# Performance work log

Hardware: AMD Instinct MI355X
Metric: run time of the kernel (lower is better)

## Reference

```python
import jax, jax.numpy as jnp
import numpy as np

C_IN = 512      # backbone feature dim (din)
CORR = 256      # cfg.SIAMESE.NUM_CHANNELS_FOR_CORRELATION
EXPAND = 64     # expand_factor
N_ANCH = 9      # 3 scales x 3 ratios
KH = 7          # template spatial size
H = W = 32      # target feature map size
N_T = 2         # number of templates
BN_EPS = 1e-5


def _conv(x, w, b=None, pad=0, groups=1):
    out = jax.lax.conv_general_dilated(
        x, w, window_strides=(1, 1), padding=[(pad, pad), (pad, pad)],
        dimension_numbers=('NCHW', 'OIHW', 'NCHW'), feature_group_count=groups)
    if b is not None:
        out = out + b[None, :, None, None]
    return out


def setup_inputs() -> dict:
    key = jax.random.key(0)
    ks = jax.random.split(key, 10)
    return {
        'target_feat': jax.random.normal(ks[0], (1, C_IN, H, W), jnp.float32),
        'template_feat': jax.random.normal(ks[1], (N_T, C_IN, KH, KH), jnp.float32),
        'w_target': jax.random.normal(ks[2], (CORR, C_IN, 3, 3), jnp.float32) * 0.01,
        'b_target': jnp.zeros((CORR,), jnp.float32),
        'bn_gamma': jnp.ones((CORR,), jnp.float32),
        'bn_beta': jnp.zeros((CORR,), jnp.float32),
        'bn_mean': jax.random.normal(ks[3], (CORR,), jnp.float32) * 0.1,
        'bn_var': jax.random.uniform(ks[4], (CORR,), jnp.float32, 0.5, 1.5),
        'w_template': jax.random.normal(ks[5], (CORR * EXPAND, C_IN, 3, 3), jnp.float32) * 0.01,
        'b_template': jnp.zeros((CORR * EXPAND,), jnp.float32),
        'w_merge_cls': jax.random.normal(ks[6], (CORR,), jnp.float32) * 0.01,
        'corr_bias': jnp.zeros((EXPAND, 1, 1), jnp.float32),
        'w_cls': jax.random.normal(ks[7], (2 * N_ANCH, EXPAND, 1, 1), jnp.float32) * 0.01,
        'b_cls': jnp.zeros((2 * N_ANCH,), jnp.float32),
        'w_box': jax.random.normal(ks[8], (4 * N_ANCH, EXPAND, 1, 1), jnp.float32) * 0.001,
        'b_box': jnp.zeros((4 * N_ANCH,), jnp.float32),
    }


def reference(target_feat, template_feat, w_target, b_target, bn_gamma, bn_beta,
              bn_mean, bn_var, w_template, b_template, w_merge_cls, corr_bias,
              w_cls, b_cls, w_box, b_box):
    N = template_feat.shape[0]
    Hh, Ww = target_feat.shape[2], target_feat.shape[3]
    # RPN_Conv_target (3x3, pad 1) + BatchNorm (eval mode, running stats)
    t = _conv(target_feat, w_target, b_target, pad=1)               # (1, CORR, H, W)
    scale = (bn_gamma / jnp.sqrt(bn_var + BN_EPS))[None, :, None, None]
    t = (t - bn_mean[None, :, None, None]) * scale + bn_beta[None, :, None, None]
    # RPN_Conv_template (3x3, pad 1) on template features
    z = _conv(template_feat, w_template, b_template, pad=1)          # (N, CORR*EXPAND, kh, kw)
    kh, kw = z.shape[2], z.shape[3]
    # depth-wise cross correlation: kernel (N*EXPAND*CORR, 1, kh, kw), groups=CORR
    kern = z.reshape(N * EXPAND * CORR, 1, kh, kw)
    out = 0.1 * _conv(t, kern, pad=(kh - 1) // 2, groups=CORR)       # (1, N*EXPAND*CORR, H, W)
    out = out.reshape(N * EXPAND, CORR, Hh, Ww)
    # conv_merge_1x1_cls: 1x1 conv CORR -> 1, no bias
    out = jnp.einsum('nchw,c->nhw', out, w_merge_cls)                # (N*EXPAND, H, W)
    rpn_feat = out.reshape(N, EXPAND, Hh, Ww) + corr_bias[None]      # (N, 64, H, W)
    # cls / bbox heads (1x1 convs)
    cls = _conv(rpn_feat, w_cls, b_cls)                              # (N, 18, H, W)
    box = _conv(rpn_feat, w_box, b_box)                              # (N, 36, H, W)
    nc = cls.shape[1]
    # reshape to (N, 2, A*H, W), softmax over dim 1, reshape back
    prob = jax.nn.softmax(cls.reshape(N, 2, (nc // 2) * Hh, Ww), axis=1)
    prob = prob.reshape(N, nc, Hh, Ww)
    return prob, box
```

## Files before the change

### kernel.cpp

```cpp
#include <hip/hip_runtime.h>
#include <math.h>


#define WS_TFP 0
#define WS_TP  591872
#define WS_BF  980992
#define WS_WFP 981120
#define WS_Z2P 2160768
#define WS_MRG 2562176
#define WS_CVP 2693248
#define WFP_HALF 589824

typedef float f4u __attribute__((ext_vector_type(4), aligned(4)));
typedef float f4a __attribute__((ext_vector_type(4)));

#define FMA4(ww, vv) \
  acc.x = fmaf(ww, (vv).x, acc.x); acc.y = fmaf(ww, (vv).y, acc.y); \
  acc.z = fmaf(ww, (vv).z, acc.z); acc.w = fmaf(ww, (vv).w, acc.w)

__global__ __launch_bounds__(256) void k0_prep(
    const float* __restrict__ tfeat,
    const float* __restrict__ wm,
    const float* __restrict__ btpl,
    float* ws)
{
  const int N0 = 591872, N2 = 389120;
  const int total = N0 + N2;
  for (int idx = blockIdx.x * 256 + threadIdx.x; idx < total + 128; idx += gridDim.x * 256) {
    if (idx < N0) {
      int ci = idx / 1156, r = idx % 1156;
      int yy = r / 34, xx = r % 34;
      float v = 0.f;
      if (yy >= 1 && yy <= 32 && xx >= 1 && xx <= 32)
        v = tfeat[ci * 1024 + (yy - 1) * 32 + (xx - 1)];
      ws[WS_TFP + idx] = v;
    } else if (idx < total) {
      ws[WS_TP + (idx - N0)] = 0.f;
    } else {
      const int eh = idx - total;
      const int e = eh >> 1, h = eh & 1;
      const float* wmp = wm + h * 128;
      const float* bp = btpl + e * 256 + h * 128;
      float s = 0.f;
      for (int cl = 0; cl < 128; cl++) s = fmaf(wmp[cl], bp[cl], s);
      ws[WS_BF + eh] = s;
    }
  }
}

__global__ __launch_bounds__(256, 8) void K1_fold_conv(
    const float* __restrict__ wtpl,
    const float* __restrict__ wm,
    const float* __restrict__ wtgt,
    float* ws)
{
  const int bid0 = blockIdx.x;
  const int tid = threadIdx.x;
  const int q = bid0 / 17, r17 = bid0 % 17;
  if (r17 < 9) {
    const int fi = q * 9 + r17;
    const int g = fi / 18, rest = fi % 18;
    const int chunk = rest >> 1, half = rest & 1;
    const int colv = tid & 127, rowg = tid >> 7;
    const int c0 = chunk * 512 + colv * 4;
    const int row0 = g * 128 + half * 64 + rowg * 32;
    const float* base = wtpl + (size_t)row0 * 4608 + c0;
    const float* wmb = wm + (g & 1) * 128 + half * 64 + rowg * 32;
    f4a acc = {0.f, 0.f, 0.f, 0.f};
    for (int rr = 0; rr < 32; rr += 8) {
      const float* b = base + (size_t)rr * 4608;
      const f4a v0 = *(const f4a*)(b);
      const f4a v1 = *(const f4a*)(b + 1 * 4608);
      const f4a v2 = *(const f4a*)(b + 2 * 4608);
      const f4a v3 = *(const f4a*)(b + 3 * 4608);
      const f4a v4 = *(const f4a*)(b + 4 * 4608);
      const f4a v5 = *(const f4a*)(b + 5 * 4608);
      const f4a v6 = *(const f4a*)(b + 6 * 4608);
      const f4a v7 = *(const f4a*)(b + 7 * 4608);
      const float w0 = wmb[rr + 0], w1 = wmb[rr + 1];
      const float w2 = wmb[rr + 2], w3 = wmb[rr + 3];
      const float w4 = wmb[rr + 4], w5 = wmb[rr + 5];
      const float w6 = wmb[rr + 6], w7 = wmb[rr + 7];
      FMA4(w0, v0); FMA4(w1, v1); FMA4(w2, v2); FMA4(w3, v3);
      FMA4(w4, v4); FMA4(w5, v5); FMA4(w6, v6); FMA4(w7, v7);
    }
    __shared__ f4a red[128];
    if (rowg) red[colv] = acc;
    __syncthreads();
    if (!rowg) {
      const f4a o = red[colv];
      acc.x += o.x; acc.y += o.y; acc.z += o.z; acc.w += o.w;
      float* wp = ws + WS_WFP + (size_t)half * WFP_HALF + (size_t)g * 4608;
      *(f4a*)(wp + c0) = acc;
    }
  } else {
    const int bid = q * 8 + (r17 - 9);
    const int coblk = bid >> 7, pxblk = (bid >> 3) & 15, ks = bid & 7;
    const int ksub = tid >> 7, sub = tid & 127;
    const int cog = sub >> 5, pxg = sub & 31;
    const int row = pxg >> 4, x0 = (pxg & 15) * 2;
    const int y = pxblk * 2 + row;
    const int co0 = coblk * 16 + cog * 4;
    const int ci0 = ks * 64 + ksub * 32;
    const float* tfp = ws + WS_TFP;

    float acc[4][2] = {{0.f, 0.f}, {0.f, 0.f}, {0.f, 0.f}, {0.f, 0.f}};
    for (int i = 0; i < 32; i++) {
      const int ci = ci0 + i;
      const float* tin = tfp + (size_t)ci * 1156 + y * 34 + x0;
      const f4u p0 = *(const f4u*)(tin);
      const f4u p1 = *(const f4u*)(tin + 34);
      const f4u p2 = *(const f4u*)(tin + 68);
      #pragma unroll
      for (int c = 0; c < 4; c++) {
        const float* wr = wtgt + (size_t)(co0 + c) * 4608 + ci * 9;
        const f4u wa = *(const f4u*)(wr);
        const f4u wb = *(const f4u*)(wr + 4);
        const float w8 = wr[8];
        acc[c][0] += wa.x * p0.x + wa.y * p0.y + wa.z * p0.z
                   + wa.w * p1.x + wb.x * p1.y + wb.y * p1.z
                   + wb.z * p2.x + wb.w * p2.y + w8 * p2.z;
        acc[c][1] += wa.x * p0.y + wa.y * p0.z + wa.z * p0.w
                   + wa.w * p1.y + wb.x * p1.z + wb.y * p1.w
                   + wb.z * p2.y + wb.w * p2.z + w8 * p2.w;
      }
    }
    float* cvp = ws + WS_CVP + (size_t)(ks * 2 + ksub) * 262144;
    #pragma unroll
    for (int c = 0; c < 4; c++) {
      cvp[(co0 + c) * 1024 + y * 32 + x0 + 0] = acc[c][0];
      cvp[(co0 + c) * 1024 + y * 32 + x0 + 1] = acc[c][1];
    }
  }
}

__global__ __launch_bounds__(256) void K2_cred_z2(
    const float* __restrict__ btgt,
    const float* __restrict__ gamma, const float* __restrict__ beta,
    const float* __restrict__ mean, const float* __restrict__ var,
    const float* __restrict__ zfeat,
    float* ws)
{
  __shared__ float Tl[50][144];
  const int tid = threadIdx.x;
  if (blockIdx.x < 256) {
    const int co = blockIdx.x;
    const float sc = gamma[co] * rsqrtf(var[co] + 1e-5f);
    const float off = btgt[co] - mean[co];
    const float bt = beta[co];
    const float* cvp = ws + WS_CVP + (size_t)co * 1024;
    float* tP = ws + WS_TP;
    #pragma unroll
    for (int k = 0; k < 4; k++) {
      const int j = k * 256 + tid;
      float s = 0.f;
      #pragma unroll
      for (int sl = 0; sl < 16; sl++) s += cvp[(size_t)sl * 262144 + j];
      const float t = ((s + off) * sc + bt) * 0.1f;
      const int yy = j >> 5, xx = j & 31;
      tP[co * 1520 + (yy + 3) * 40 + (xx + 3)] = t;
    }
  } else {
    const int b2 = blockIdx.x - 256;
    const int n = b2 >> 5, kc = b2 & 31;
    const int ci0 = kc * 16;
    for (int idx = tid; idx < 7200; idx += 256) {
      const int uv = idx / 144, kk = idx % 144;
      float v = 0.f;
      if (uv < 49) {
        const int u = uv / 7, vv = uv % 7;
        const int ci = ci0 + kk / 9, pq = kk % 9;
        const int p = pq / 3, q2 = pq % 3;
        const int yy = u + p - 1, xx = vv + q2 - 1;
        if (yy >= 0 && yy < 7 && xx >= 0 && xx < 7)
          v = zfeat[n * 25088 + ci * 49 + yy * 7 + xx];
      }
      Tl[uv][kk] = v;
    }
    __syncthreads();
    const int ehq = tid & 31, uvg = tid >> 5;
    const int eh0 = ehq * 4;
    const int uv0 = (uvg == 0) ? 0 : uvg * 6 + 1;
    const float* wfp = ws + WS_WFP;
    float4 acc[7];
    #pragma unroll
    for (int i = 0; i < 7; i++) acc[i] = make_float4(0.f, 0.f, 0.f, 0.f);
    for (int g = 0; g < 36; g++) {
      const int koff = ci0 * 9 + g * 4;
      f4a wvE[4];
      #pragma unroll
      for (int e = 0; e < 4; e++) {
        const float* pe = wfp + (size_t)(eh0 + e) * 4608 + koff;
        f4a a = *(const f4a*)(pe);
        a += *(const f4a*)(pe + WFP_HALF);
        wvE[e] = a;
      }
      #pragma unroll
      for (int uu = 0; uu < 7; uu++) {
        const float4 t4 = *(const float4*)(&Tl[uv0 + uu][g * 4]);
        acc[uu].x = fmaf(t4.x, wvE[0].x, fmaf(t4.y, wvE[0].y, fmaf(t4.z, wvE[0].z, fmaf(t4.w, wvE[0].w, acc[uu].x))));
        acc[uu].y = fmaf(t4.x, wvE[1].x, fmaf(t4.y, wvE[1].y, fmaf(t4.z, wvE[1].z, fmaf(t4.w, wvE[1].w, acc[uu].y))));
        acc[uu].z = fmaf(t4.x, wvE[2].x, fmaf(t4.y, wvE[2].y, fmaf(t4.z, wvE[2].z, fmaf(t4.w, wvE[2].w, acc[uu].z))));
        acc[uu].w = fmaf(t4.x, wvE[3].x, fmaf(t4.y, wvE[3].y, fmaf(t4.z, wvE[3].z, fmaf(t4.w, wvE[3].w, acc[uu].w))));
      }
    }
    float* z2p = ws + WS_Z2P;
    #pragma unroll
    for (int uu = 0; uu < 7; uu++) {
      const int uv = uv0 + uu;
      if (uv <= 48)
        *(float4*)(z2p + ((size_t)((n * 32 + kc) * 49 + uv)) * 128 + eh0) = acc[uu];
    }
  }
}

__global__ __launch_bounds__(128) void k3_merged(float* ws)
{
  __shared__ float Z2s[16][7][8];
  const int tid = threadIdx.x;
  const int bid = blockIdx.x;
  const int n = bid >> 7, rest = bid & 127;
  const int ec = rest >> 4, hq = rest & 15;
  const int c0 = ec * 16, h0 = hq * 2;
  const float* z2p = ws + WS_Z2P;
  const float* bf = ws + WS_BF;
  for (int idx = tid; idx < 784; idx += 128) {
    const int cl = idx & 15, uv = idx >> 4;
    float s = bf[c0 + cl];
    const float* p = z2p + (size_t)(n * 1568 + uv) * 128 + (c0 + cl);
    #pragma unroll 8
    for (int kc = 0; kc < 32; kc++) s += p[(size_t)kc * 6272];
    Z2s[cl][uv / 7][uv % 7] = s;
  }
  for (int idx = tid; idx < 112; idx += 128)
    Z2s[idx / 7][idx % 7][7] = 0.f;
  __syncthreads();

  const int e = tid >> 4, row = (tid >> 3) & 1, wq = tid & 7;
  const int w0 = wq * 4;
  const float* tP = ws + WS_TP;
  float acc[4] = {0.f, 0.f, 0.f, 0.f};
  #pragma unroll
  for (int h128 = 0; h128 < 2; h128++) {
    const int cl = 2 * e + h128;
    const float* tc = tP + (size_t)(128 * n + c0 + cl) * 1520;
    #pragma unroll
    for (int u = 0; u < 7; u++) {
      const float* trow = tc + (h0 + row + u) * 40 + w0;
      float tw[12];
      *(float4*)&tw[0] = *(const float4*)(trow);
      *(float4*)&tw[4] = *(const float4*)(trow + 4);
      *(float4*)&tw[8] = *(const float4*)(trow + 8);
      float z[8];
      *(float4*)&z[0] = *(const float4*)&Z2s[cl][u][0];
      *(float4*)&z[4] = *(const float4*)&Z2s[cl][u][4];
      #pragma unroll
      for (int px = 0; px < 4; px++)
        #pragma unroll
        for (int v = 0; v < 8; v++)
          acc[px] = fmaf(z[v], tw[px + v], acc[px]);
    }
  }
  float* mrg = ws + WS_MRG;
  *(float4*)(mrg + (size_t)(((n * 64 + ec * 8 + e) * 32) + h0 + row) * 32 + w0) =
      make_float4(acc[0], acc[1], acc[2], acc[3]);
}

__global__ __launch_bounds__(256) void k4_heads(
    const float* __restrict__ cb,
    const float* __restrict__ wcls, const float* __restrict__ bcls,
    const float* __restrict__ wbox, const float* __restrict__ bbox,
    float* ws, float* __restrict__ out)
{
  __shared__ float mrg_l[32][66];
  __shared__ float wcb_l[54][64];
  __shared__ float bias_l[54];
  __shared__ float logits[18][32];
  const int tid = threadIdx.x;
  const int n = blockIdx.x >> 5, h = blockIdx.x & 31;
  const float* mrg = ws + WS_MRG;
  for (int idx = tid; idx < 2048; idx += 256) {
    const int e = idx >> 5, w = idx & 31;
    mrg_l[w][e] = mrg[(size_t)(((n * 64 + e) * 32) + h) * 32 + w] + cb[e];
  }
  for (int idx = tid; idx < 3456; idx += 256) {
    const int ch = idx >> 6, e = idx & 63;
    wcb_l[ch][e] = (ch < 18) ? wcls[ch * 64 + e] : wbox[(ch - 18) * 64 + e];
  }
  if (tid < 54) bias_l[tid] = (tid < 18) ? bcls[tid] : bbox[tid - 18];
  __syncthreads();

  const int w = tid & 31, chg = tid >> 5;
  const int cnt = (chg < 6) ? 7 : 6;
  float acc[7] = {0.f, 0.f, 0.f, 0.f, 0.f, 0.f, 0.f};
  for (int e2 = 0; e2 < 32; e2++) {
    const float2 m2 = *(const float2*)&mrg_l[w][e2 * 2];
    #pragma unroll
    for (int i = 0; i < 7; i++) {
      if (i < cnt) {
        const int ch = chg + 8 * i;
        const float2 wv = *(const float2*)&wcb_l[ch][e2 * 2];
        acc[i] = fmaf(m2.x, wv.x, acc[i]);
        acc[i] = fmaf(m2.y, wv.y, acc[i]);
      }
    }
  }
  #pragma unroll
  for (int i = 0; i < 7; i++) {
    if (i < cnt) {
      const int ch = chg + 8 * i;
      const float v = acc[i] + bias_l[ch];
      if (ch < 18) logits[ch][w] = v;
      else out[36864 + n * 36864 + (ch - 18) * 1024 + h * 32 + w] = v;
    }
  }
  __syncthreads();
  for (int idx = tid; idx < 576; idx += 256) {
    const int ch = idx >> 5, w2 = idx & 31;
    const float a = logits[ch][w2];
    const float b = logits[(ch + 9) % 18][w2];
    const float m = fmaxf(a, b);
    const float ea = expf(a - m), eb = expf(b - m);
    out[n * 18432 + ch * 1024 + h * 32 + w2] = ea / (ea + eb);
  }
}

extern "C" void kernel_launch(void* const* d_in, const int* in_sizes, int n_in,
                              void* d_out, int out_size, void* d_ws, size_t ws_size,
                              hipStream_t stream) {
  (void)in_sizes; (void)n_in; (void)out_size; (void)ws_size;
  const float* target_feat   = (const float*)d_in[0];
  const float* template_feat = (const float*)d_in[1];
  const float* w_target      = (const float*)d_in[2];
  const float* b_target      = (const float*)d_in[3];
  const float* bn_gamma      = (const float*)d_in[4];
  const float* bn_beta       = (const float*)d_in[5];
  const float* bn_mean       = (const float*)d_in[6];
  const float* bn_var        = (const float*)d_in[7];
  const float* w_template    = (const float*)d_in[8];
  const float* b_template    = (const float*)d_in[9];
  const float* w_merge       = (const float*)d_in[10];
  const float* corr_bias     = (const float*)d_in[11];
  const float* w_cls         = (const float*)d_in[12];
  const float* b_cls         = (const float*)d_in[13];
  const float* w_box         = (const float*)d_in[14];
  const float* b_box         = (const float*)d_in[15];
  float* ws = (float*)d_ws;
  float* out = (float*)d_out;

  hipLaunchKernelGGL(k0_prep, dim3(2048), dim3(256), 0, stream,
                     target_feat, w_merge, b_template, ws);
  hipLaunchKernelGGL(K1_fold_conv, dim3(4352), dim3(256), 0, stream,
                     w_template, w_merge, w_target, ws);
  hipLaunchKernelGGL(K2_cred_z2, dim3(320), dim3(256), 0, stream,
                     b_target, bn_gamma, bn_beta, bn_mean, bn_var,
                     template_feat, ws);
  hipLaunchKernelGGL(k3_merged, dim3(256), dim3(128), 0, stream, ws);
  hipLaunchKernelGGL(k4_heads, dim3(64), dim3(256), 0, stream,
                     corr_bias, w_cls, b_cls, w_box, b_box, ws, out);
}
```

Baseline: 240.2 us.

## Split fold into standalone wide kernel with 8 partial slabs and nontemporal loads

The template-weight fold that merges w_merge into w_template moves out of the combined fold/conv kernel into its own kernel. That kernel launches 9216 blocks, each reducing 16 rows and writing one of 8 partial slabs, where before fewer blocks each looped over 64 rows. The big weight stream now uses nontemporal loads, and the conv part becomes its own kernel. The goal is more memory-level parallelism on the large w_template read. In exchange, K2 must sum 8 slabs instead of 2 on every weight load, the workspace grows, and there is one more kernel launch.

```diff
diff --git a/kernel.cpp b/kernel.cpp
--- a/kernel.cpp
+++ b/kernel.cpp
@@ -6,10 +6,10 @@
 #define WS_TP  591872
 #define WS_BF  980992
 #define WS_WFP 981120
-#define WS_Z2P 2160768
-#define WS_MRG 2562176
-#define WS_CVP 2693248
-#define WFP_HALF 589824
+#define WS_Z2P 5699712
+#define WS_MRG 6101120
+#define WS_CVP 6232192
+#define WFP_SLAB 589824
 
 typedef float f4u __attribute__((ext_vector_type(4), aligned(4)));
 typedef float f4a __attribute__((ext_vector_type(4)));
@@ -17,6 +17,46 @@
 #define FMA4(ww, vv) \
   acc.x = fmaf(ww, (vv).x, acc.x); acc.y = fmaf(ww, (vv).y, acc.y); \
   acc.z = fmaf(ww, (vv).z, acc.z); acc.w = fmaf(ww, (vv).w, acc.w)
+
+#define NTL(p) __builtin_nontemporal_load((const f4a*)(p))
+
+__global__ __launch_bounds__(256) void k_fold(
+    const float* __restrict__ wtpl,
+    const float* __restrict__ wm,
+    float* ws)
+{
+  const int b = blockIdx.x;
+  const int g = b / 72, rest = b % 72;
+  const int chunk = rest / 8, rsub = rest % 8;
+  const int tid = threadIdx.x;
+  const int colv = tid & 127, rowg = tid >> 7;
+  const int c0 = chunk * 512 + colv * 4;
+  const int row0 = g * 128 + rsub * 16 + rowg * 8;
+  const float* base = wtpl + (size_t)row0 * 4608 + c0;
+  const float* wmb = wm + (g & 1) * 128 + rsub * 16 + rowg * 8;
+  f4a acc = {0.f, 0.f, 0.f, 0.f};
+  const f4a v0 = NTL(base);
+  const f4a v1 = NTL(base + 1 * 4608);
+  const f4a v2 = NTL(base + 2 * 4608);
+  const f4a v3 = NTL(base + 3 * 4608);
+  const f4a v4 = NTL(base + 4 * 4608);
+  const f4a v5 = NTL(base + 5 * 4608);
+  const f4a v6 = NTL(base + 6 * 4608);
+  const f4a v7 = NTL(base + 7 * 4608);
+  const float w0 = wmb[0], w1 = wmb[1], w2 = wmb[2], w3 = wmb[3];
+  const float w4 = wmb[4], w5 = wmb[5], w6 = wmb[6], w7 = wmb[7];
+  FMA4(w0, v0); FMA4(w1, v1); FMA4(w2, v2); FMA4(w3, v3);
+  FMA4(w4, v4); FMA4(w5, v5); FMA4(w6, v6); FMA4(w7, v7);
+  __shared__ f4a red[128];
+  if (rowg) red[colv] = acc;
+  __syncthreads();
+  if (!rowg) {
+    const f4a o = red[colv];
+    acc.x += o.x; acc.y += o.y; acc.z += o.z; acc.w += o.w;
+    float* wp = ws + WS_WFP + (size_t)rsub * WFP_SLAB + (size_t)g * 4608;
+    *(f4a*)(wp + c0) = acc;
+  }
+}
 
 __global__ __launch_bounds__(256) void k0_prep(
     const float* __restrict__ tfeat,
@@ -48,89 +88,47 @@
   }
 }
 
-__global__ __launch_bounds__(256, 8) void K1_fold_conv(
-    const float* __restrict__ wtpl,
-    const float* __restrict__ wm,
+__global__ __launch_bounds__(256) void k_conv(
     const float* __restrict__ wtgt,
     float* ws)
 {
-  const int bid0 = blockIdx.x;
-  const int tid = threadIdx.x;
-  const int q = bid0 / 17, r17 = bid0 % 17;
-  if (r17 < 9) {
-    const int fi = q * 9 + r17;
-    const int g = fi / 18, rest = fi % 18;
-    const int chunk = rest >> 1, half = rest & 1;
-    const int colv = tid & 127, rowg = tid >> 7;
-    const int c0 = chunk * 512 + colv * 4;
-    const int row0 = g * 128 + half * 64 + rowg * 32;
-    const float* base = wtpl + (size_t)row0 * 4608 + c0;
-    const float* wmb = wm + (g & 1) * 128 + half * 64 + rowg * 32;
-    f4a acc = {0.f, 0.f, 0.f, 0.f};
-    for (int rr = 0; rr < 32; rr += 8) {
-      const float* b = base + (size_t)rr * 4608;
-      const f4a v0 = *(const f4a*)(b);
-      const f4a v1 = *(const f4a*)(b + 1 * 4608);
-      const f4a v2 = *(const f4a*)(b + 2 * 4608);
-      const f4a v3 = *(const f4a*)(b + 3 * 4608);
-      const f4a v4 = *(const f4a*)(b + 4 * 4608);
-      const f4a v5 = *(const f4a*)(b + 5 * 4608);
-      const f4a v6 = *(const f4a*)(b + 6 * 4608);
-      const f4a v7 = *(const f4a*)(b + 7 * 4608);
-      const float w0 = wmb[rr + 0], w1 = wmb[rr + 1];
-      const float w2 = wmb[rr + 2], w3 = wmb[rr + 3];
-      const float w4 = wmb[rr + 4], w5 = wmb[rr + 5];
-      const float w6 = wmb[rr + 6], w7 = wmb[rr + 7];
-      FMA4(w0, v0); FMA4(w1, v1); FMA4(w2, v2); FMA4(w3, v3);
-      FMA4(w4, v4); FMA4(w5, v5); FMA4(w6, v6); FMA4(w7, v7);
-    }
-    __shared__ f4a red[128];
-    if (rowg) red[colv] = acc;
-    __syncthreads();
-    if (!rowg) {
-      const f4a o = red[colv];
-      acc.x += o.x; acc.y += o.y; acc.z += o.z; acc.w += o.w;
-      float* wp = ws + WS_WFP + (size_t)half * WFP_HALF + (size_t)g * 4608;
-      *(f4a*)(wp + c0) = acc;
-    }
-  } else {
-    const int bid = q * 8 + (r17 - 9);
-    const int coblk = bid >> 7, pxblk = (bid >> 3) & 15, ks = bid & 7;
-    const int ksub = tid >> 7, sub = tid & 127;
-    const int cog = sub >> 5, pxg = sub & 31;
-    const int row = pxg >> 4, x0 = (pxg & 15) * 2;
-    const int y = pxblk * 2 + row;
-    const int co0 = coblk * 16 + cog * 4;
-    const int ci0 = ks * 64 + ksub * 32;
-    const float* tfp = ws + WS_TFP;
-
-    float acc[4][2] = {{0.f, 0.f}, {0.f, 0.f}, {0.f, 0.f}, {0.f, 0.f}};
-    for (int i = 0; i < 32; i++) {
-      const int ci = ci0 + i;
-      const float* tin = tfp + (size_t)ci * 1156 + y * 34 + x0;
-      const f4u p0 = *(const f4u*)(tin);
-      const f4u p1 = *(const f4u*)(tin + 34);
-      const f4u p2 = *(const f4u*)(tin + 68);
-      #pragma unroll
-      for (int c = 0; c < 4; c++) {
-        const float* wr = wtgt + (size_t)(co0 + c) * 4608 + ci * 9;
-        const f4u wa = *(const f4u*)(wr);
-        const f4u wb = *(const f4u*)(wr + 4);
-        const float w8 = wr[8];
-        acc[c][0] += wa.x * p0.x + wa.y * p0.y + wa.z * p0.z
-                   + wa.w * p1.x + wb.x * p1.y + wb.y * p1.z
-                   + wb.z * p2.x + wb.w * p2.y + w8 * p2.z;
-        acc[c][1] += wa.x * p0.y + wa.y * p0.z + wa.z * p0.w
-                   + wa.w * p1.y + wb.x * p1.z + wb.y * p1.w
-                   + wb.z * p2.y + wb.w * p2.z + w8 * p2.w;
-      }
-    }
-    float* cvp = ws + WS_CVP + (size_t)(ks * 2 + ksub) * 262144;
+  const int bid = blockIdx.x;
+  const int coblk = bid >> 7, pxblk = (bid >> 3) & 15, ks = bid & 7;
+  const int tid = threadIdx.x;
+  const int ksub = tid >> 7, sub = tid & 127;
+  const int cog = sub >> 5, pxg = sub & 31;
+  const int row = pxg >> 4, x0 = (pxg & 15) * 2;
+  const int y = pxblk * 2 + row;
+  const int co0 = coblk * 16 + cog * 4;
+  const int ci0 = ks * 64 + ksub * 32;
+  const float* tfp = ws + WS_TFP;
+
+  float acc[4][2] = {{0.f, 0.f}, {0.f, 0.f}, {0.f, 0.f}, {0.f, 0.f}};
+  for (int i = 0; i < 32; i++) {
+    const int ci = ci0 + i;
+    const float* tin = tfp + (size_t)ci * 1156 + y * 34 + x0;
+    const f4u p0 = *(const f4u*)(tin);
+    const f4u p1 = *(const f4u*)(tin + 34);
+    const f4u p2 = *(const f4u*)(tin + 68);
     #pragma unroll
     for (int c = 0; c < 4; c++) {
-      cvp[(co0 + c) * 1024 + y * 32 + x0 + 0] = acc[c][0];
-      cvp[(co0 + c) * 1024 + y * 32 + x0 + 1] = acc[c][1];
-    }
+      const float* wr = wtgt + (size_t)(co0 + c) * 4608 + ci * 9;
+      const f4u wa = *(const f4u*)(wr);
+      const f4u wb = *(const f4u*)(wr + 4);
+      const float w8 = wr[8];
+      acc[c][0] += wa.x * p0.x + wa.y * p0.y + wa.z * p0.z
+                 + wa.w * p1.x + wb.x * p1.y + wb.y * p1.z
+                 + wb.z * p2.x + wb.w * p2.y + w8 * p2.z;
+      acc[c][1] += wa.x * p0.y + wa.y * p0.z + wa.z * p0.w
+                 + wa.w * p1.y + wb.x * p1.z + wb.y * p1.w
+                 + wb.z * p2.y + wb.w * p2.z + w8 * p2.w;
+    }
+  }
+  float* cvp = ws + WS_CVP + (size_t)(ks * 2 + ksub) * 262144;
+  #pragma unroll
+  for (int c = 0; c < 4; c++) {
+    cvp[(co0 + c) * 1024 + y * 32 + x0 + 0] = acc[c][0];
+    cvp[(co0 + c) * 1024 + y * 32 + x0 + 1] = acc[c][1];
   }
 }
 
@@ -192,7 +190,9 @@
       for (int e = 0; e < 4; e++) {
         const float* pe = wfp + (size_t)(eh0 + e) * 4608 + koff;
         f4a a = *(const f4a*)(pe);
-        a += *(const f4a*)(pe + WFP_HALF);
+        #pragma unroll
+        for (int sl = 1; sl < 8; sl++)
+          a += *(const f4a*)(pe + (size_t)sl * WFP_SLAB);
         wvE[e] = a;
       }
       #pragma unroll
@@ -348,10 +348,12 @@
   float* ws = (float*)d_ws;
   float* out = (float*)d_out;
 
+  hipLaunchKernelGGL(k_fold, dim3(9216), dim3(256), 0, stream,
+                     w_template, w_merge, ws);
   hipLaunchKernelGGL(k0_prep, dim3(2048), dim3(256), 0, stream,
                      target_feat, w_merge, b_template, ws);
-  hipLaunchKernelGGL(K1_fold_conv, dim3(4352), dim3(256), 0, stream,
-                     w_template, w_merge, w_target, ws);
+  hipLaunchKernelGGL(k_conv, dim3(2048), dim3(256), 0, stream,
+                     w_target, ws);
   hipLaunchKernelGGL(K2_cred_z2, dim3(320), dim3(256), 0, stream,
                      b_target, bn_gamma, bn_beta, bn_mean, bn_var,
                      template_feat, ws);
```

Measured after the change: 333.8 us. 39.0% more time.
